# Kernel optimization log

Hardware: AMD Instinct MI355X
Metric: run time of the kernel (lower is better)

Reference implementation:

```python
import math
import jax, jax.numpy as jnp
import numpy as np

B, S, D, H, HD = 32, 512, 768, 12, 64
K, ST = 2, 2  # pooling kernel / stride
NEG = jnp.float32(-10000.0)


def _alibi_slopes(n):
    def p2(m):
        start = 2 ** (-(2 ** (-(math.log2(m) - 3))))
        return [start * start ** i for i in range(m)]
    if math.log2(n).is_integer():
        return p2(n)
    c = 2 ** math.floor(math.log2(n))
    return p2(c) + _alibi_slopes(2 * c)[0::2][: n - c]


def _sum_pool(x, k, s, out_len):
    # x: [B, L, C]; ceil_mode sum-pool over axis 1 (zero padded on the right)
    pad = (out_len - 1) * s + k - x.shape[1]
    if pad > 0:
        x = jnp.pad(x, ((0, 0), (0, pad), (0, 0)))
    win = x[:, jnp.arange(out_len)[:, None] * s + jnp.arange(k)]  # [B, out, k, C]
    return win.sum(axis=2)


def setup_inputs() -> dict:
    key = jax.random.key(0)
    k1, k2, k3 = jax.random.split(key, 3)
    hidden_states = jax.random.normal(k1, (B, S, D), dtype=jnp.float32)
    lengths = jax.random.randint(k2, (B,), 128, S + 1)
    attention_mask = jnp.arange(S)[None, :] < lengths[:, None]  # bool [B,S]
    Wqkv_w = jax.random.normal(k3, (3 * D, D), dtype=jnp.float32) * 0.02
    Wqkv_b = jnp.zeros((3 * D,), dtype=jnp.float32)
    return {"hidden_states": hidden_states, "attention_mask": attention_mask,
            "Wqkv_w": Wqkv_w, "Wqkv_b": Wqkv_b}


def reference(hidden_states, attention_mask, Wqkv_w, Wqkv_b):
    b, s = attention_mask.shape
    qkv = hidden_states @ Wqkv_w.T + Wqkv_b  # [B,S,3D]
    qkv = qkv.reshape(b, s, 3, H, HD)        # '(t h d)' split order
    q = qkv[:, :, 0]                          # [B,S,H,HD]
    k = qkv[:, :, 1].transpose(0, 2, 1, 3)    # [B,H,S,HD]
    v = qkv[:, :, 2].transpose(0, 2, 1, 3)

    # MaskedAvgPool1d on queries (flattened heads), ceil_mode sum-pool / count
    kk = min(K, s)
    out_len = -(-(max(0, s - kk)) // ST) + 1
    q_flat = q.reshape(b, s, H * HD)
    q_flat = jnp.where(attention_mask[:, :, None], q_flat, 0.0)
    norm = _sum_pool(attention_mask.astype(jnp.float32)[:, :, None], kk, ST, out_len)  # [B,out,1]
    new_mask = norm[..., 0] != 0
    norm = jnp.where(norm == 0, 1.0, norm)
    q_pool = _sum_pool(q_flat, kk, ST, out_len) / norm  # [B,out,D]
    q = q_pool.reshape(b, out_len, H, HD).transpose(0, 2, 1, 3)  # [B,H,out,HD]

    # bias: 0 where (new_mask_q & mask_k), else -10000; plus ALiBi
    pair = new_mask[:, :, None] & attention_mask[:, None, :]  # [B,out,S]
    bias = jnp.where(pair, 0.0, NEG)[:, None, :, :]           # [B,1,out,S]
    rel = jnp.abs(jnp.arange(s)[None, :] - jnp.arange(out_len)[:, None])  # [out,S]
    slopes = jnp.asarray(_alibi_slopes(H), dtype=jnp.float32)
    alibi = slopes[:, None, None] * (-rel.astype(jnp.float32))  # [H,out,S]
    scores = jnp.einsum('bhqd,bhkd->bhqk', q, k) / math.sqrt(HD) + bias + alibi[None]
    attn = jax.nn.softmax(scores, axis=-1)
    out = jnp.einsum('bhqk,bhkd->bhqd', attn, v)  # [B,H,out,HD]
    out = out.transpose(0, 2, 1, 3).reshape(b, out_len, H * HD)
    return out, new_mask
```

## Files before the change

### kernel.cpp

```cpp
#include <hip/hip_runtime.h>

#define BB 32
#define SS 512
#define DD 768
#define HH 12
#define HDIM 64
#define OL 256
#define NQKV 2304
#define GM (BB*SS)

#define NEG2 (-14426.9504089f)

typedef __bf16 bf16_t;
typedef bf16_t bf16x8 __attribute__((ext_vector_type(8)));
typedef float f32x4 __attribute__((ext_vector_type(4)));
typedef unsigned short u16x8 __attribute__((ext_vector_type(8)));

__device__ __forceinline__ unsigned short f2bf(float f) {
  unsigned u = __float_as_uint(f);
  u = u + 0x7FFFu + ((u >> 16) & 1u);
  return (unsigned short)(u >> 16);
}
__device__ __forceinline__ float b2f(unsigned short s) {
  return __uint_as_float(((unsigned)s) << 16);
}

__global__ void conv_f32_bf16(const float* __restrict__ in,
                              unsigned short* __restrict__ out, int n4) {
  int i = blockIdx.x * blockDim.x + threadIdx.x;
  if (i >= n4) return;
  float4 v = ((const float4*)in)[i];
  ushort4 o;
  o.x = f2bf(v.x); o.y = f2bf(v.y); o.z = f2bf(v.z); o.w = f2bf(v.w);
  ((ushort4*)out)[i] = o;
}

__global__ void prep_mask(const void* __restrict__ mraw,
                          float* __restrict__ kbias,
                          float* __restrict__ invn,
                          unsigned char* __restrict__ nmask,
                          float* __restrict__ out_nm) {
  int b = blockIdx.x, t = threadIdx.x;
  const unsigned char* mb = (const unsigned char*)mraw;
  bool isbyte = (mb[1] != 0);
  int idx = b * SS + t;
  int mv = isbyte ? (int)(mb[idx] != 0) : (int)(((const int*)mraw)[idx] != 0);
  kbias[idx] = mv ? 0.f : NEG2;
  if (t < OL) {
    int i0 = b * SS + 2 * t, i1 = i0 + 1;
    int m0 = isbyte ? (int)(mb[i0] != 0) : (int)(((const int*)mraw)[i0] != 0);
    int m1 = isbyte ? (int)(mb[i1] != 0) : (int)(((const int*)mraw)[i1] != 0);
    int n = m0 + m1;
    invn[b * OL + t] = (n > 0) ? 1.f / (float)n : 1.f;
    nmask[b * OL + t] = (n > 0) ? 1 : 0;
    out_nm[b * OL + t] = (n > 0) ? 1.f : 0.f;
  }
}

#define NT 12
__global__ __launch_bounds__(256, 2) void gemm_qkv(
    const unsigned short* __restrict__ A,
    const unsigned short* __restrict__ Bt,
    const float* __restrict__ bias,
    unsigned short* __restrict__ Kbuf,
    unsigned short* __restrict__ qp,
    unsigned short* __restrict__ vT,
    const float* __restrict__ kbias,
    const float* __restrict__ invn) {
  __shared__ __align__(16) char smem[65536];

  const int t = threadIdx.x;
  const int lane = t & 63;
  const int w = t >> 6;
  const int wm = w >> 1, wn = w & 1;
  const int fr = lane & 15, hi = lane >> 4;

  const int p = blockIdx.x;
  const int l = (p & 7) * 288 + (p >> 3);
  const int m0 = (l / 18) * 128;
  const int n0 = (l % 18) * 128;
  const int b = m0 >> 9;
  const int s0 = m0 & 511;

  f32x4 acc[4][4] = {};

  const int sr8 = lane >> 3;
  const int sx8 = ((lane & 7) ^ sr8) * 8;
  const int wq = __builtin_amdgcn_readfirstlane(w);
  const unsigned short* aSrc = A + (size_t)(m0 + wq * 32 + sr8) * DD + sx8;
  const unsigned short* bSrc = Bt + (size_t)(n0 + wq * 32 + sr8) * DD + sx8;

#define GLOAD(SRC, DST)                                                        \
  __builtin_amdgcn_global_load_lds(                                           \
      (const __attribute__((address_space(1))) unsigned int*)(SRC),           \
      (__attribute__((address_space(3))) unsigned int*)(DST), 16, 0, 0)

#define STAGE(T) do {                                                          \
    char* da_ = smem + ((T) & 1) * 32768;                                      \
    char* db_ = da_ + 16384;                                                   \
    const unsigned short* as_ = aSrc + (T) * 64;                               \
    const unsigned short* bs_ = bSrc + (T) * 64;                               \
    _Pragma("unroll")                                                          \
    for (int i_ = 0; i_ < 4; ++i_) {                                           \
      GLOAD(as_ + (size_t)i_ * 8 * DD, da_ + (wq * 32 + i_ * 8) * 128);        \
      GLOAD(bs_ + (size_t)i_ * 8 * DD, db_ + (wq * 32 + i_ * 8) * 128);        \
    }                                                                          \
  } while (0)

  STAGE(0);
  STAGE(1);

  const int cb0 = (hi * 16) ^ ((fr & 7) << 4);
  const int cb1 = (64 + hi * 16) ^ ((fr & 7) << 4);

  for (int kt = 0; kt < NT; ++kt) {
    if (kt < NT - 1) {
      asm volatile("s_waitcnt vmcnt(8)" ::: "memory");
    } else {
      asm volatile("s_waitcnt vmcnt(0)" ::: "memory");
    }
    __builtin_amdgcn_sched_barrier(0);
    __builtin_amdgcn_s_barrier();
    __builtin_amdgcn_sched_barrier(0);

    const char* bA = smem + (kt & 1) * 32768;
    const char* bB = bA + 16384;

    bf16x8 a0[4], b0[4], a1[4], b1[4];
#pragma unroll
    for (int f = 0; f < 4; ++f) {
      a0[f] = *(const bf16x8*)(bA + (wm * 64 + f * 16 + fr) * 128 + cb0);
      b0[f] = *(const bf16x8*)(bB + (wn * 64 + f * 16 + fr) * 128 + cb0);
    }
    __builtin_amdgcn_sched_barrier(0);
#pragma unroll
    for (int f = 0; f < 4; ++f) {
      a1[f] = *(const bf16x8*)(bA + (wm * 64 + f * 16 + fr) * 128 + cb1);
      b1[f] = *(const bf16x8*)(bB + (wn * 64 + f * 16 + fr) * 128 + cb1);
    }
    asm volatile("s_waitcnt lgkmcnt(8)" ::: "memory");
    __builtin_amdgcn_sched_barrier(0);
    __builtin_amdgcn_s_setprio(1);
#pragma unroll
    for (int mf = 0; mf < 4; ++mf)
#pragma unroll
      for (int nf = 0; nf < 4; ++nf)
        acc[mf][nf] = __builtin_amdgcn_mfma_f32_16x16x32_bf16(
            a0[mf], b0[nf], acc[mf][nf], 0, 0, 0);
    __builtin_amdgcn_s_setprio(0);
    asm volatile("s_waitcnt lgkmcnt(0)" ::: "memory");
    __builtin_amdgcn_sched_barrier(0);
    __builtin_amdgcn_s_barrier();
    __builtin_amdgcn_sched_barrier(0);
    if (kt + 2 < NT) STAGE(kt + 2);
    __builtin_amdgcn_sched_barrier(0);
    __builtin_amdgcn_s_setprio(1);
#pragma unroll
    for (int mf = 0; mf < 4; ++mf)
#pragma unroll
      for (int nf = 0; nf < 4; ++nf)
        acc[mf][nf] = __builtin_amdgcn_mfma_f32_16x16x32_bf16(
            a1[mf], b1[nf], acc[mf][nf], 0, 0, 0);
    __builtin_amdgcn_s_setprio(0);
  }
#undef STAGE
#undef GLOAD

  const int ntype = n0 / 768;
  if (ntype == 1) {
#pragma unroll
    for (int nf = 0; nf < 4; ++nf) {
      const int nc = wn * 64 + nf * 16 + fr;
      const float bvs = bias[n0 + nc];
      const int gnc = n0 - 768 + nc;
#pragma unroll
      for (int mf = 0; mf < 4; ++mf) {
        const int gmr = m0 + wm * 64 + mf * 16 + hi * 4;
#pragma unroll
        for (int j = 0; j < 4; ++j)
          Kbuf[(size_t)(gmr + j) * 768 + gnc] = f2bf(acc[mf][nf][j] + bvs);
      }
    }
  } else if (ntype == 0) {
#pragma unroll
    for (int mf = 0; mf < 4; ++mf) {
      const int sl = s0 + wm * 64 + mf * 16 + hi * 4;
      const float4 km = *(const float4*)&kbias[b * SS + sl];
      const float2 iv = *(const float2*)&invn[b * OL + (sl >> 1)];
      const float w0 = (km.x == 0.f) ? iv.x : 0.f;
      const float w1 = (km.y == 0.f) ? iv.x : 0.f;
      const float w2 = (km.z == 0.f) ? iv.y : 0.f;
      const float w3 = (km.w == 0.f) ? iv.y : 0.f;
      const int o0 = b * OL + (sl >> 1);
#pragma unroll
      for (int nf = 0; nf < 4; ++nf) {
        const int gnc = n0 + wn * 64 + nf * 16 + fr;
        const float bvs = bias[gnc];
        const f32x4 a = acc[mf][nf];
        qp[(size_t)o0 * DD + gnc] = f2bf((a[0] + bvs) * w0 + (a[1] + bvs) * w1);
        qp[(size_t)(o0 + 1) * DD + gnc] = f2bf((a[2] + bvs) * w2 + (a[3] + bvs) * w3);
      }
    }
  } else {
    unsigned short* lt = (unsigned short*)smem;
#pragma unroll
    for (int nf = 0; nf < 4; ++nf) {
      const int nl = wn * 64 + nf * 16 + fr;
      const float bvs = bias[n0 + nl];
#pragma unroll
      for (int mf = 0; mf < 4; ++mf) {
        const int mb = wm * 64 + mf * 16 + hi * 4;
        ushort4 pk;
        pk.x = f2bf(acc[mf][nf][0] + bvs);
        pk.y = f2bf(acc[mf][nf][1] + bvs);
        pk.z = f2bf(acc[mf][nf][2] + bvs);
        pk.w = f2bf(acc[mf][nf][3] + bvs);
        *(ushort4*)&lt[nl * 136 + mb] = pk;
      }
    }
    __syncthreads();
#pragma unroll
    for (int i = 0; i < 8; ++i) {
      const int row = i * 16 + (t >> 4);
      const int ch = t & 15;
      const u16x8 v = *(const u16x8*)&lt[row * 136 + ch * 8];
      const int n = n0 - 1536 + row;
      const int h2 = n >> 6, d2 = n & 63;
      *(u16x8*)(vT + ((size_t)((b * HH + h2) * HDIM + d2)) * 512 + s0 + ch * 8) = v;
    }
  }
}

__constant__ float c_slopes2[12] = {
    0.72134752f, 0.36067376f, 0.18033688f, 0.09016844f,
    0.04508422f, 0.02254211f, 0.011271055f, 0.0056355275f,
    1.02013945f, 0.51006972f, 0.25503486f, 0.12751743f};

__global__ __launch_bounds__(256) void attn_mfma(
    const unsigned short* __restrict__ qp,
    const unsigned short* __restrict__ Kb,
    const unsigned short* __restrict__ vT,
    const float* __restrict__ kbias,
    const unsigned char* __restrict__ nmask,
    float* __restrict__ out) {
  __shared__ __align__(16) char smem[51200];
  const int t = threadIdx.x;
  const int lane = t & 63;
  const int w = t >> 6;
  const int wq = __builtin_amdgcn_readfirstlane(w);
  const int fr = lane & 15, hi = lane >> 4;

  const int p = blockIdx.x;
  const int l = (p & 7) * 96 + (p >> 3);
  const int qb = l & 1;
  const int bh = l >> 1;
  const int h = bh % HH, b = bh / HH;
  const int q0 = qb * 128 + wq * 32;

  char* ptb = smem + 32768 + wq * 4096;
  float* kbl = (float*)(smem + 49152);

  const int srow = lane >> 3;
  const int scol = ((lane & 7) ^ srow) * 8;

#define GLOAD(SRC, DST)                                                        \
  __builtin_amdgcn_global_load_lds(                                           \
      (const __attribute__((address_space(1))) unsigned int*)(SRC),           \
      (__attribute__((address_space(3))) unsigned int*)(DST), 16, 0, 0)

  if (wq == 0) {
    GLOAD(kbias + b * SS + lane * 4, smem + 49152);
    GLOAD(kbias + b * SS + 256 + lane * 4, smem + 50176);
  }

  bf16x8 qf[2][2];
#pragma unroll
  for (int m = 0; m < 2; ++m)
#pragma unroll
    for (int ks = 0; ks < 2; ++ks)
      qf[m][ks] = *(const bf16x8*)(qp + (size_t)(b * OL + q0 + m * 16 + fr) * DD +
                                   h * HDIM + ks * 32 + hi * 8);

  int nmv = (int)nmask[b * OL + q0 + (lane & 31)];
  int qmbits = 0;
#pragma unroll
  for (int m = 0; m < 2; ++m)
#pragma unroll
    for (int j = 0; j < 4; ++j)
      if (__shfl(nmv, m * 16 + hi * 4 + j, 64)) qmbits |= 1 << (m * 4 + j);

  const float slope2 = c_slopes2[h];
  f32x4 oacc[2][4] = {};
  float lpart[2][4] = {};

#define STAGE(TILE, BUF) do {                                                  \
    char* kd_ = smem + (BUF) * 8192 + wq * 2048;                               \
    char* vd_ = smem + 16384 + (BUF) * 8192 + wq * 2048;                       \
    const unsigned short* ks_ =                                                \
        Kb + (size_t)(b * SS + (TILE) * 64 + wq * 16 + srow) * 768 + h * HDIM + scol; \
    const unsigned short* vs_ =                                                \
        vT + (size_t)((b * HH + h) * HDIM + wq * 16 + srow) * SS + (TILE) * 64 + scol; \
    GLOAD(ks_, kd_);                                                           \
    GLOAD(ks_ + (size_t)8 * 768, kd_ + 1024);                                  \
    GLOAD(vs_, vd_);                                                           \
    GLOAD(vs_ + (size_t)8 * SS, vd_ + 1024);                                   \
  } while (0)

  __builtin_amdgcn_sched_barrier(0);
  STAGE(0, 0);
  STAGE(1, 1);
  __builtin_amdgcn_sched_barrier(0);

  for (int tile = 0; tile < 8; ++tile) {
    const int cur = tile & 1;
    const int key0 = tile * 64;
    if (tile < 7) {
      asm volatile("s_waitcnt vmcnt(4)" ::: "memory");
    } else {
      asm volatile("s_waitcnt vmcnt(0)" ::: "memory");
    }
    __builtin_amdgcn_sched_barrier(0);
    __builtin_amdgcn_s_barrier();
    __builtin_amdgcn_sched_barrier(0);

    char* ktb = smem + cur * 8192;
    char* vtb = smem + 16384 + cur * 8192;

    f32x4 sacc[2][4] = {};
#pragma unroll
    for (int ks = 0; ks < 2; ++ks) {
      bf16x8 kf[4];
#pragma unroll
      for (int n = 0; n < 4; ++n) {
        const int by = ((n * 16 + fr) * 128 + (ks * 64 + hi * 16)) ^ ((fr & 7) << 4);
        kf[n] = *(const bf16x8*)(ktb + by);
      }
#pragma unroll
      for (int m = 0; m < 2; ++m)
#pragma unroll
        for (int n = 0; n < 4; ++n)
          sacc[m][n] = __builtin_amdgcn_mfma_f32_16x16x32_bf16(qf[m][ks], kf[n], sacc[m][n], 0, 0, 0);
    }

    float kbv[4], keyfv[4];
#pragma unroll
    for (int n = 0; n < 4; ++n) {
      kbv[n] = kbl[key0 + n * 16 + fr];
      keyfv[n] = (float)(key0 + n * 16 + fr);
    }
#pragma unroll
    for (int m = 0; m < 2; ++m) {
#pragma unroll
      for (int j = 0; j < 4; ++j) {
        const bool qm = (qmbits >> (m * 4 + j)) & 1;
        const float qvf = (float)(q0 + m * 16 + hi * 4 + j);
        float lp = lpart[m][j];
#pragma unroll
        for (int n = 0; n < 4; ++n) {
          const float biasv = qm ? kbv[n] : 0.f;
          const float rel = fabsf(keyfv[n] - qvf);
          float tv = fmaf(sacc[m][n][j], 0.18033688011f, biasv);
          tv = fmaf(rel, -slope2, tv);
          float pe;
          asm("v_exp_f32 %0, %1" : "=v"(pe) : "v"(tv));
          lp += pe;
          const int by = ((m * 16 + hi * 4 + j) * 128 + (n * 16 + fr) * 2) ^
                         (((hi * 4 + j) & 7) << 4);
          *(unsigned short*)(ptb + by) = f2bf(pe);
        }
        lpart[m][j] = lp;
      }
    }
    asm volatile("s_waitcnt lgkmcnt(0)" ::: "memory");
    __builtin_amdgcn_sched_barrier(0);

#pragma unroll
    for (int ks = 0; ks < 2; ++ks) {
      bf16x8 pf[2], vf[4];
#pragma unroll
      for (int m = 0; m < 2; ++m) {
        const int by = ((m * 16 + fr) * 128 + (ks * 64 + hi * 16)) ^ ((fr & 7) << 4);
        pf[m] = *(const bf16x8*)(ptb + by);
      }
#pragma unroll
      for (int nd = 0; nd < 4; ++nd) {
        const int by = ((nd * 16 + fr) * 128 + (ks * 64 + hi * 16)) ^ ((fr & 7) << 4);
        vf[nd] = *(const bf16x8*)(vtb + by);
      }
#pragma unroll
      for (int m = 0; m < 2; ++m)
#pragma unroll
        for (int nd = 0; nd < 4; ++nd)
          oacc[m][nd] = __builtin_amdgcn_mfma_f32_16x16x32_bf16(pf[m], vf[nd], oacc[m][nd], 0, 0, 0);
    }

    __builtin_amdgcn_sched_barrier(0);
    __builtin_amdgcn_s_barrier();
    __builtin_amdgcn_sched_barrier(0);
    if (tile + 2 < 8) STAGE(tile + 2, cur);
  }
#undef STAGE
#undef GLOAD

  float* ot = (float*)(smem + wq * 8704);
#pragma unroll
  for (int m = 0; m < 2; ++m)
#pragma unroll
    for (int j = 0; j < 4; ++j) {
      float lv = lpart[m][j];
      lv += __shfl_xor(lv, 1, 64);
      lv += __shfl_xor(lv, 2, 64);
      lv += __shfl_xor(lv, 4, 64);
      lv += __shfl_xor(lv, 8, 64);
      const float rl = 1.f / lv;
      const int row = m * 16 + hi * 4 + j;
#pragma unroll
      for (int nd = 0; nd < 4; ++nd)
        ot[row * 68 + nd * 16 + fr] = oacc[m][nd][j] * rl;
    }
  asm volatile("s_waitcnt lgkmcnt(0)" ::: "memory");
  __builtin_amdgcn_sched_barrier(0);
#pragma unroll
  for (int i = 0; i < 8; ++i) {
    const int idx = i * 64 + lane;
    const int row = idx >> 4, c4 = idx & 15;
    const float4 v = *(const float4*)&ot[row * 68 + c4 * 4];
    *(float4*)(out + (size_t)(b * OL + q0 + row) * DD + h * HDIM + c4 * 4) = v;
  }
}

extern "C" void kernel_launch(void* const* d_in, const int* in_sizes, int n_in,
                              void* d_out, int out_size, void* d_ws, size_t ws_size,
                              hipStream_t stream) {
  const float* hidden = (const float*)d_in[0];
  const void* maskraw = d_in[1];
  const float* W = (const float*)d_in[2];
  const float* bias = (const float*)d_in[3];
  float* out = (float*)d_out;

  char* ws = (char*)d_ws;
  unsigned short* Abf  = (unsigned short*)(ws);
  unsigned short* Btb  = (unsigned short*)(ws + 25165824);
  unsigned short* Kbuf = (unsigned short*)(ws + 28704768);
  unsigned short* vT   = (unsigned short*)(ws + 53870592);
  unsigned short* qp   = (unsigned short*)(ws + 79036416);
  float* kbias         = (float*)(ws + 91619328);
  float* invn          = (float*)(ws + 91684864);
  unsigned char* nmask = (unsigned char*)(ws + 91717632);

  float* out_nm = out + (size_t)BB * OL * DD;

  conv_f32_bf16<<<(GM * DD / 4 + 255) / 256, 256, 0, stream>>>(hidden, Abf, GM * DD / 4);
  conv_f32_bf16<<<(NQKV * DD / 4 + 255) / 256, 256, 0, stream>>>(W, Btb, NQKV * DD / 4);
  prep_mask<<<BB, SS, 0, stream>>>(maskraw, kbias, invn, nmask, out_nm);
  gemm_qkv<<<2304, 256, 0, stream>>>(Abf, Btb, bias, Kbuf, qp, vT, kbias, invn);
  attn_mfma<<<768, 256, 0, stream>>>(qp, Kbuf, vT, kbias, nmask, out);
}
```

Before: 112.3 us.

## Enlarge QKV GEMM tile to 128x256 with 8 waves and triple-buffered LDS

The QKV projection GEMM now uses 512-thread blocks, each computing a 128x256 output tile with a 2x4 wave grid, so half as many blocks are launched. Global-to-LDS staging moves from double to triple buffering across 144 KB of shared memory. Each K-step's loads are split into two halves interleaved between the MFMA phases, with waits tuned to match. The goal is better operand reuse per loaded byte and better overlap of memory traffic with MFMA work. In exchange, the large LDS footprint likely limits residency to one block per CU, and tile-level parallelism drops.

```diff
diff --git a/kernel.cpp b/kernel.cpp
--- a/kernel.cpp
+++ b/kernel.cpp
@@ -57,8 +57,7 @@
   }
 }
 
-#define NT 12
-__global__ __launch_bounds__(256, 2) void gemm_qkv(
+__global__ __launch_bounds__(512, 2) void gemm_qkv(
     const unsigned short* __restrict__ A,
     const unsigned short* __restrict__ Bt,
     const float* __restrict__ bias,
@@ -67,18 +66,19 @@
     unsigned short* __restrict__ vT,
     const float* __restrict__ kbias,
     const float* __restrict__ invn) {
-  __shared__ __align__(16) char smem[65536];
+  __shared__ __align__(16) char smem[147456];
 
   const int t = threadIdx.x;
   const int lane = t & 63;
   const int w = t >> 6;
-  const int wm = w >> 1, wn = w & 1;
+  const int wm = w >> 2;
+  const int wn = w & 3;
   const int fr = lane & 15, hi = lane >> 4;
 
   const int p = blockIdx.x;
-  const int l = (p & 7) * 288 + (p >> 3);
-  const int m0 = (l / 18) * 128;
-  const int n0 = (l % 18) * 128;
+  const int l = (p & 7) * 144 + (p >> 3);
+  const int m0 = (l / 9) * 128;
+  const int n0 = (l % 9) * 256;
   const int b = m0 >> 9;
   const int s0 = m0 & 511;
 
@@ -87,87 +87,111 @@
   const int sr8 = lane >> 3;
   const int sx8 = ((lane & 7) ^ sr8) * 8;
   const int wq = __builtin_amdgcn_readfirstlane(w);
-  const unsigned short* aSrc = A + (size_t)(m0 + wq * 32 + sr8) * DD + sx8;
-  const unsigned short* bSrc = Bt + (size_t)(n0 + wq * 32 + sr8) * DD + sx8;
+  const unsigned short* aS = A + (size_t)(m0 + wq * 16 + sr8) * DD + sx8;
+  const unsigned short* bS = Bt + (size_t)(n0 + wq * 32 + sr8) * DD + sx8;
 
 #define GLOAD(SRC, DST)                                                        \
   __builtin_amdgcn_global_load_lds(                                           \
       (const __attribute__((address_space(1))) unsigned int*)(SRC),           \
       (__attribute__((address_space(3))) unsigned int*)(DST), 16, 0, 0)
 
-#define STAGE(T) do {                                                          \
-    char* da_ = smem + ((T) & 1) * 32768;                                      \
-    char* db_ = da_ + 16384;                                                   \
-    const unsigned short* as_ = aSrc + (T) * 64;                               \
-    const unsigned short* bs_ = bSrc + (T) * 64;                               \
+#define STG_A(KT, SB, Q) GLOAD(aS + (size_t)(8 * (Q)) * DD + (KT) * 64,        \
+                               (SB) + (wq * 16 + 8 * (Q)) * 128)
+#define STG_B(KT, SB, Q) GLOAD(bS + (size_t)(8 * (Q)) * DD + (KT) * 64,        \
+                               (SB) + 16384 + (wq * 32 + 8 * (Q)) * 128)
+#define STG_H1(KT, SB) do { STG_A(KT, SB, 0); STG_A(KT, SB, 1); STG_B(KT, SB, 0); } while (0)
+#define STG_H2(KT, SB) do { STG_B(KT, SB, 1); STG_B(KT, SB, 2); STG_B(KT, SB, 3); } while (0)
+
+#define SBAR()                                                                 \
+  do {                                                                         \
+    __builtin_amdgcn_sched_barrier(0);                                         \
+    __builtin_amdgcn_s_barrier();                                              \
+    __builtin_amdgcn_sched_barrier(0);                                         \
+  } while (0)
+
+#define MFMA16(AF, BF)                                                         \
+  do {                                                                         \
+    asm volatile("s_waitcnt lgkmcnt(0)" ::: "memory");                          \
+    __builtin_amdgcn_sched_barrier(0);                                         \
+    __builtin_amdgcn_s_setprio(1);                                             \
     _Pragma("unroll")                                                          \
-    for (int i_ = 0; i_ < 4; ++i_) {                                           \
-      GLOAD(as_ + (size_t)i_ * 8 * DD, da_ + (wq * 32 + i_ * 8) * 128);        \
-      GLOAD(bs_ + (size_t)i_ * 8 * DD, db_ + (wq * 32 + i_ * 8) * 128);        \
-    }                                                                          \
+    for (int mf_ = 0; mf_ < 4; ++mf_)                                          \
+      _Pragma("unroll")                                                        \
+      for (int nf_ = 0; nf_ < 4; ++nf_)                                        \
+        acc[mf_][nf_] = __builtin_amdgcn_mfma_f32_16x16x32_bf16(               \
+            (AF)[mf_], (BF)[nf_], acc[mf_][nf_], 0, 0, 0);                     \
+    __builtin_amdgcn_s_setprio(0);                                             \
   } while (0)
-
-  STAGE(0);
-  STAGE(1);
 
   const int cb0 = (hi * 16) ^ ((fr & 7) << 4);
   const int cb1 = (64 + hi * 16) ^ ((fr & 7) << 4);
-
-  for (int kt = 0; kt < NT; ++kt) {
-    if (kt < NT - 1) {
-      asm volatile("s_waitcnt vmcnt(8)" ::: "memory");
+  const int arow = (wm * 64 + fr) * 128;
+  const int brow = 16384 + (wn * 64 + fr) * 128;
+
+  STG_H1(0, smem); STG_H2(0, smem);
+  STG_H1(1, smem + 49152); STG_H2(1, smem + 49152);
+
+  int se = 0;
+#pragma unroll
+  for (int it = 0; it < 6; ++it) {
+    char* sE = smem + se * 49152;
+    char* sO = smem + (se == 2 ? 0 : se + 1) * 49152;
+    char* dE = smem + (se == 0 ? 2 : se - 1) * 49152;
+    char* dO = sE;
+    const int ke = 2 * it + 2, ko = 2 * it + 3;
+
+    bf16x8 af[4], bf[4];
+
+    asm volatile("s_waitcnt vmcnt(6)" ::: "memory");
+    SBAR();
+#pragma unroll
+    for (int f = 0; f < 4; ++f) af[f] = *(const bf16x8*)(sE + arow + f * 2048 + cb0);
+#pragma unroll
+    for (int f = 0; f < 4; ++f) bf[f] = *(const bf16x8*)(sE + brow + f * 2048 + cb0);
+    if (it < 5) STG_H1(ke, dE);
+    MFMA16(af, bf);
+
+    SBAR();
+#pragma unroll
+    for (int f = 0; f < 4; ++f) af[f] = *(const bf16x8*)(sE + arow + f * 2048 + cb1);
+#pragma unroll
+    for (int f = 0; f < 4; ++f) bf[f] = *(const bf16x8*)(sE + brow + f * 2048 + cb1);
+    if (it < 5) STG_H2(ke, dE);
+    MFMA16(af, bf);
+
+    if (it < 5) {
+      asm volatile("s_waitcnt vmcnt(6)" ::: "memory");
     } else {
       asm volatile("s_waitcnt vmcnt(0)" ::: "memory");
     }
-    __builtin_amdgcn_sched_barrier(0);
-    __builtin_amdgcn_s_barrier();
-    __builtin_amdgcn_sched_barrier(0);
-
-    const char* bA = smem + (kt & 1) * 32768;
-    const char* bB = bA + 16384;
-
-    bf16x8 a0[4], b0[4], a1[4], b1[4];
-#pragma unroll
-    for (int f = 0; f < 4; ++f) {
-      a0[f] = *(const bf16x8*)(bA + (wm * 64 + f * 16 + fr) * 128 + cb0);
-      b0[f] = *(const bf16x8*)(bB + (wn * 64 + f * 16 + fr) * 128 + cb0);
-    }
-    __builtin_amdgcn_sched_barrier(0);
-#pragma unroll
-    for (int f = 0; f < 4; ++f) {
-      a1[f] = *(const bf16x8*)(bA + (wm * 64 + f * 16 + fr) * 128 + cb1);
-      b1[f] = *(const bf16x8*)(bB + (wn * 64 + f * 16 + fr) * 128 + cb1);
-    }
-    asm volatile("s_waitcnt lgkmcnt(8)" ::: "memory");
-    __builtin_amdgcn_sched_barrier(0);
-    __builtin_amdgcn_s_setprio(1);
-#pragma unroll
-    for (int mf = 0; mf < 4; ++mf)
-#pragma unroll
-      for (int nf = 0; nf < 4; ++nf)
-        acc[mf][nf] = __builtin_amdgcn_mfma_f32_16x16x32_bf16(
-            a0[mf], b0[nf], acc[mf][nf], 0, 0, 0);
-    __builtin_amdgcn_s_setprio(0);
-    asm volatile("s_waitcnt lgkmcnt(0)" ::: "memory");
-    __builtin_amdgcn_sched_barrier(0);
-    __builtin_amdgcn_s_barrier();
-    __builtin_amdgcn_sched_barrier(0);
-    if (kt + 2 < NT) STAGE(kt + 2);
-    __builtin_amdgcn_sched_barrier(0);
-    __builtin_amdgcn_s_setprio(1);
-#pragma unroll
-    for (int mf = 0; mf < 4; ++mf)
-#pragma unroll
-      for (int nf = 0; nf < 4; ++nf)
-        acc[mf][nf] = __builtin_amdgcn_mfma_f32_16x16x32_bf16(
-            a1[mf], b1[nf], acc[mf][nf], 0, 0, 0);
-    __builtin_amdgcn_s_setprio(0);
-  }
-#undef STAGE
+    SBAR();
+#pragma unroll
+    for (int f = 0; f < 4; ++f) af[f] = *(const bf16x8*)(sO + arow + f * 2048 + cb0);
+#pragma unroll
+    for (int f = 0; f < 4; ++f) bf[f] = *(const bf16x8*)(sO + brow + f * 2048 + cb0);
+    if (it < 5) STG_H1(ko, dO);
+    MFMA16(af, bf);
+
+    SBAR();
+#pragma unroll
+    for (int f = 0; f < 4; ++f) af[f] = *(const bf16x8*)(sO + arow + f * 2048 + cb1);
+#pragma unroll
+    for (int f = 0; f < 4; ++f) bf[f] = *(const bf16x8*)(sO + brow + f * 2048 + cb1);
+    if (it < 5) STG_H2(ko, dO);
+    MFMA16(af, bf);
+
+    se = (se + 2) % 3;
+  }
+#undef STG_A
+#undef STG_B
+#undef STG_H1
+#undef STG_H2
+#undef MFMA16
+#undef SBAR
 #undef GLOAD
 
-  const int ntype = n0 / 768;
-  if (ntype == 1) {
+  const int nt = n0 / 768;
+  if (nt == 1) {
 #pragma unroll
     for (int nf = 0; nf < 4; ++nf) {
       const int nc = wn * 64 + nf * 16 + fr;
@@ -181,7 +205,7 @@
           Kbuf[(size_t)(gmr + j) * 768 + gnc] = f2bf(acc[mf][nf][j] + bvs);
       }
     }
-  } else if (ntype == 0) {
+  } else if (nt == 0) {
 #pragma unroll
     for (int mf = 0; mf < 4; ++mf) {
       const int sl = s0 + wm * 64 + mf * 16 + hi * 4;
@@ -209,23 +233,24 @@
       const float bvs = bias[n0 + nl];
 #pragma unroll
       for (int mf = 0; mf < 4; ++mf) {
-        const int mb = wm * 64 + mf * 16 + hi * 4;
+        const int ml = wm * 64 + mf * 16 + hi * 4;
         ushort4 pk;
         pk.x = f2bf(acc[mf][nf][0] + bvs);
         pk.y = f2bf(acc[mf][nf][1] + bvs);
         pk.z = f2bf(acc[mf][nf][2] + bvs);
         pk.w = f2bf(acc[mf][nf][3] + bvs);
-        *(ushort4*)&lt[nl * 136 + mb] = pk;
+        *(ushort4*)&lt[nl * 136 + ml] = pk;
       }
     }
     __syncthreads();
 #pragma unroll
     for (int i = 0; i < 8; ++i) {
-      const int row = i * 16 + (t >> 4);
-      const int ch = t & 15;
-      const u16x8 v = *(const u16x8*)&lt[row * 136 + ch * 8];
-      const int n = n0 - 1536 + row;
-      const int h2 = n >> 6, d2 = n & 63;
+      const int task = i * 512 + t;
+      const int r = task >> 4;
+      const int ch = task & 15;
+      const u16x8 v = *(const u16x8*)&lt[r * 136 + ch * 8];
+      const int nv = n0 - 1536 + r;
+      const int h2 = nv >> 6, d2 = nv & 63;
       *(u16x8*)(vT + ((size_t)((b * HH + h2) * HDIM + d2)) * 512 + s0 + ch * 8) = v;
     }
   }
@@ -453,6 +478,6 @@
   conv_f32_bf16<<<(GM * DD / 4 + 255) / 256, 256, 0, stream>>>(hidden, Abf, GM * DD / 4);
   conv_f32_bf16<<<(NQKV * DD / 4 + 255) / 256, 256, 0, stream>>>(W, Btb, NQKV * DD / 4);
   prep_mask<<<BB, SS, 0, stream>>>(maskraw, kbias, invn, nmask, out_nm);
-  gemm_qkv<<<2304, 256, 0, stream>>>(Abf, Btb, bias, Kbuf, qp, vT, kbias, invn);
+  gemm_qkv<<<1152, 512, 0, stream>>>(Abf, Btb, bias, Kbuf, qp, vT, kbias, invn);
   attn_mfma<<<768, 256, 0, stream>>>(qp, Kbuf, vT, kbias, nmask, out);
 }
```

After: 114.8 us. 2.2% more time.

## Enlarge QKV GEMM tile to 256x256 with 8 waves and per-wave V transpose

Applied to the files above, without the earlier changes.

The QKV projection GEMM moves from 128x128 tiles with 4 waves to 256x256 tiles with 8 waves (512 threads, 128KB LDS double buffer). Each wave now computes 128x64, which raises arithmetic intensity and cuts global/LDS traffic per FLOP. The V-transpose epilogue is redone per wave through a private LDS tile, so it no longer needs a block-wide sync. In exchange the grid drops to 576 blocks and there is more register pressure (32 accumulators), which may lower occupancy and hurt load balance across CUs. With 128KB of LDS per block, the __launch_bounds__(512, 2) hint likely cannot be met, so probably only one block fits per CU.

```diff
diff --git a/kernel.cpp b/kernel.cpp
--- a/kernel.cpp
+++ b/kernel.cpp
@@ -57,8 +57,7 @@
   }
 }
 
-#define NT 12
-__global__ __launch_bounds__(256, 2) void gemm_qkv(
+__global__ __launch_bounds__(512, 2) void gemm_qkv(
     const unsigned short* __restrict__ A,
     const unsigned short* __restrict__ Bt,
     const float* __restrict__ bias,
@@ -67,54 +66,80 @@
     unsigned short* __restrict__ vT,
     const float* __restrict__ kbias,
     const float* __restrict__ invn) {
-  __shared__ __align__(16) char smem[65536];
+  __shared__ __align__(16) char smem[131072];
 
   const int t = threadIdx.x;
   const int lane = t & 63;
   const int w = t >> 6;
-  const int wm = w >> 1, wn = w & 1;
+  const int wm = w >> 2;
+  const int wn = w & 3;
   const int fr = lane & 15, hi = lane >> 4;
 
   const int p = blockIdx.x;
-  const int l = (p & 7) * 288 + (p >> 3);
-  const int m0 = (l / 18) * 128;
-  const int n0 = (l % 18) * 128;
+  const int l = (p & 7) * 72 + (p >> 3);
+  const int m0 = (l / 9) * 256;
+  const int n0 = (l % 9) * 256;
   const int b = m0 >> 9;
   const int s0 = m0 & 511;
 
-  f32x4 acc[4][4] = {};
+  f32x4 acc[8][4] = {};
 
   const int sr8 = lane >> 3;
   const int sx8 = ((lane & 7) ^ sr8) * 8;
   const int wq = __builtin_amdgcn_readfirstlane(w);
-  const unsigned short* aSrc = A + (size_t)(m0 + wq * 32 + sr8) * DD + sx8;
-  const unsigned short* bSrc = Bt + (size_t)(n0 + wq * 32 + sr8) * DD + sx8;
+  const unsigned short* aS = A + (size_t)(m0 + wq * 32 + sr8) * DD + sx8;
+  const unsigned short* bS = Bt + (size_t)(n0 + wq * 32 + sr8) * DD + sx8;
 
 #define GLOAD(SRC, DST)                                                        \
   __builtin_amdgcn_global_load_lds(                                           \
       (const __attribute__((address_space(1))) unsigned int*)(SRC),           \
       (__attribute__((address_space(3))) unsigned int*)(DST), 16, 0, 0)
 
-#define STAGE(T) do {                                                          \
-    char* da_ = smem + ((T) & 1) * 32768;                                      \
-    char* db_ = da_ + 16384;                                                   \
-    const unsigned short* as_ = aSrc + (T) * 64;                               \
-    const unsigned short* bs_ = bSrc + (T) * 64;                               \
+#define STAGE(KT, BUF) do {                                                    \
+    char* da_ = (BUF);                                                         \
+    char* db_ = (BUF) + 32768;                                                 \
+    const unsigned short* as_ = aS + (KT) * 64;                                \
+    const unsigned short* bs_ = bS + (KT) * 64;                                \
     _Pragma("unroll")                                                          \
-    for (int i_ = 0; i_ < 4; ++i_) {                                           \
-      GLOAD(as_ + (size_t)i_ * 8 * DD, da_ + (wq * 32 + i_ * 8) * 128);        \
-      GLOAD(bs_ + (size_t)i_ * 8 * DD, db_ + (wq * 32 + i_ * 8) * 128);        \
+    for (int q_ = 0; q_ < 4; ++q_) {                                           \
+      GLOAD(as_ + (size_t)(8 * q_) * DD, da_ + (wq * 32 + 8 * q_) * 128);      \
+      GLOAD(bs_ + (size_t)(8 * q_) * DD, db_ + (wq * 32 + 8 * q_) * 128);      \
     }                                                                          \
   } while (0)
 
-  STAGE(0);
-  STAGE(1);
+#define MFMA32()                                                               \
+  do {                                                                         \
+    asm volatile("s_waitcnt lgkmcnt(0)" ::: "memory");                          \
+    __builtin_amdgcn_sched_barrier(0);                                         \
+    __builtin_amdgcn_s_setprio(1);                                             \
+    _Pragma("unroll")                                                          \
+    for (int mf_ = 0; mf_ < 8; ++mf_)                                          \
+      _Pragma("unroll")                                                        \
+      for (int nf_ = 0; nf_ < 4; ++nf_)                                        \
+        acc[mf_][nf_] = __builtin_amdgcn_mfma_f32_16x16x32_bf16(               \
+            af[mf_], bf[nf_], acc[mf_][nf_], 0, 0, 0);                         \
+    __builtin_amdgcn_s_setprio(0);                                             \
+  } while (0)
+
+#define RD(SB, CB)                                                             \
+  do {                                                                         \
+    _Pragma("unroll")                                                          \
+    for (int f_ = 0; f_ < 8; ++f_)                                             \
+      af[f_] = *(const bf16x8*)((SB) + (wm * 128 + f_ * 16 + fr) * 128 + (CB)); \
+    _Pragma("unroll")                                                          \
+    for (int f_ = 0; f_ < 4; ++f_)                                             \
+      bf[f_] = *(const bf16x8*)((SB) + 32768 + (wn * 64 + f_ * 16 + fr) * 128 + (CB)); \
+  } while (0)
 
   const int cb0 = (hi * 16) ^ ((fr & 7) << 4);
   const int cb1 = (64 + hi * 16) ^ ((fr & 7) << 4);
 
-  for (int kt = 0; kt < NT; ++kt) {
-    if (kt < NT - 1) {
+  STAGE(0, smem);
+  STAGE(1, smem + 65536);
+
+#pragma unroll 2
+  for (int kt = 0; kt < 12; ++kt) {
+    if (kt < 11) {
       asm volatile("s_waitcnt vmcnt(8)" ::: "memory");
     } else {
       asm volatile("s_waitcnt vmcnt(0)" ::: "memory");
@@ -123,68 +148,52 @@
     __builtin_amdgcn_s_barrier();
     __builtin_amdgcn_sched_barrier(0);
 
-    const char* bA = smem + (kt & 1) * 32768;
-    const char* bB = bA + 16384;
-
-    bf16x8 a0[4], b0[4], a1[4], b1[4];
-#pragma unroll
-    for (int f = 0; f < 4; ++f) {
-      a0[f] = *(const bf16x8*)(bA + (wm * 64 + f * 16 + fr) * 128 + cb0);
-      b0[f] = *(const bf16x8*)(bB + (wn * 64 + f * 16 + fr) * 128 + cb0);
-    }
-    __builtin_amdgcn_sched_barrier(0);
-#pragma unroll
-    for (int f = 0; f < 4; ++f) {
-      a1[f] = *(const bf16x8*)(bA + (wm * 64 + f * 16 + fr) * 128 + cb1);
-      b1[f] = *(const bf16x8*)(bB + (wn * 64 + f * 16 + fr) * 128 + cb1);
-    }
-    asm volatile("s_waitcnt lgkmcnt(8)" ::: "memory");
+    char* bA = smem + (kt & 1) * 65536;
+    bf16x8 af[8], bf[4];
+
+    RD(bA, cb0);
+    MFMA32();
+
+    RD(bA, cb1);
+    asm volatile("s_waitcnt lgkmcnt(0)" ::: "memory");
+    __builtin_amdgcn_sched_barrier(0);
+    __builtin_amdgcn_s_barrier();
+    __builtin_amdgcn_sched_barrier(0);
+    if (kt + 2 < 12) STAGE(kt + 2, bA);
     __builtin_amdgcn_sched_barrier(0);
     __builtin_amdgcn_s_setprio(1);
 #pragma unroll
-    for (int mf = 0; mf < 4; ++mf)
+    for (int mf = 0; mf < 8; ++mf)
 #pragma unroll
       for (int nf = 0; nf < 4; ++nf)
         acc[mf][nf] = __builtin_amdgcn_mfma_f32_16x16x32_bf16(
-            a0[mf], b0[nf], acc[mf][nf], 0, 0, 0);
+            af[mf], bf[nf], acc[mf][nf], 0, 0, 0);
     __builtin_amdgcn_s_setprio(0);
-    asm volatile("s_waitcnt lgkmcnt(0)" ::: "memory");
-    __builtin_amdgcn_sched_barrier(0);
-    __builtin_amdgcn_s_barrier();
-    __builtin_amdgcn_sched_barrier(0);
-    if (kt + 2 < NT) STAGE(kt + 2);
-    __builtin_amdgcn_sched_barrier(0);
-    __builtin_amdgcn_s_setprio(1);
-#pragma unroll
-    for (int mf = 0; mf < 4; ++mf)
-#pragma unroll
-      for (int nf = 0; nf < 4; ++nf)
-        acc[mf][nf] = __builtin_amdgcn_mfma_f32_16x16x32_bf16(
-            a1[mf], b1[nf], acc[mf][nf], 0, 0, 0);
-    __builtin_amdgcn_s_setprio(0);
-  }
+  }
+#undef RD
+#undef MFMA32
 #undef STAGE
 #undef GLOAD
 
-  const int ntype = n0 / 768;
-  if (ntype == 1) {
+  const int nt = n0 / 768;
+  if (nt == 1) {
 #pragma unroll
     for (int nf = 0; nf < 4; ++nf) {
       const int nc = wn * 64 + nf * 16 + fr;
       const float bvs = bias[n0 + nc];
       const int gnc = n0 - 768 + nc;
 #pragma unroll
-      for (int mf = 0; mf < 4; ++mf) {
-        const int gmr = m0 + wm * 64 + mf * 16 + hi * 4;
+      for (int mf = 0; mf < 8; ++mf) {
+        const int gmr = m0 + wm * 128 + mf * 16 + hi * 4;
 #pragma unroll
         for (int j = 0; j < 4; ++j)
           Kbuf[(size_t)(gmr + j) * 768 + gnc] = f2bf(acc[mf][nf][j] + bvs);
       }
     }
-  } else if (ntype == 0) {
-#pragma unroll
-    for (int mf = 0; mf < 4; ++mf) {
-      const int sl = s0 + wm * 64 + mf * 16 + hi * 4;
+  } else if (nt == 0) {
+#pragma unroll
+    for (int mf = 0; mf < 8; ++mf) {
+      const int sl = s0 + wm * 128 + mf * 16 + hi * 4;
       const float4 km = *(const float4*)&kbias[b * SS + sl];
       const float2 iv = *(const float2*)&invn[b * OL + (sl >> 1)];
       const float w0 = (km.x == 0.f) ? iv.x : 0.f;
@@ -202,31 +211,39 @@
       }
     }
   } else {
-    unsigned short* lt = (unsigned short*)smem;
-#pragma unroll
-    for (int nf = 0; nf < 4; ++nf) {
-      const int nl = wn * 64 + nf * 16 + fr;
-      const float bvs = bias[n0 + nl];
-#pragma unroll
-      for (int mf = 0; mf < 4; ++mf) {
-        const int mb = wm * 64 + mf * 16 + hi * 4;
-        ushort4 pk;
-        pk.x = f2bf(acc[mf][nf][0] + bvs);
-        pk.y = f2bf(acc[mf][nf][1] + bvs);
-        pk.z = f2bf(acc[mf][nf][2] + bvs);
-        pk.w = f2bf(acc[mf][nf][3] + bvs);
-        *(ushort4*)&lt[nl * 136 + mb] = pk;
-      }
-    }
-    __syncthreads();
-#pragma unroll
-    for (int i = 0; i < 8; ++i) {
-      const int row = i * 16 + (t >> 4);
-      const int ch = t & 15;
-      const u16x8 v = *(const u16x8*)&lt[row * 136 + ch * 8];
-      const int n = n0 - 1536 + row;
-      const int h2 = n >> 6, d2 = n & 63;
-      *(u16x8*)(vT + ((size_t)((b * HH + h2) * HDIM + d2)) * 512 + s0 + ch * 8) = v;
+    const int h2 = ((n0 - 1536) >> 6) + wn;
+    unsigned short* tile = (unsigned short*)(smem + wq * 9216);
+    float bvs[4];
+#pragma unroll
+    for (int nf = 0; nf < 4; ++nf) bvs[nf] = bias[n0 + wn * 64 + nf * 16 + fr];
+#pragma unroll
+    for (int mh = 0; mh < 2; ++mh) {
+#pragma unroll
+      for (int nf = 0; nf < 4; ++nf) {
+        const int d = nf * 16 + fr;
+#pragma unroll
+        for (int mf2 = 0; mf2 < 4; ++mf2) {
+          const int mf = mh * 4 + mf2;
+          ushort4 pk;
+          pk.x = f2bf(acc[mf][nf][0] + bvs[nf]);
+          pk.y = f2bf(acc[mf][nf][1] + bvs[nf]);
+          pk.z = f2bf(acc[mf][nf][2] + bvs[nf]);
+          pk.w = f2bf(acc[mf][nf][3] + bvs[nf]);
+          *(ushort4*)&tile[d * 72 + mf2 * 16 + hi * 4] = pk;
+        }
+      }
+      asm volatile("s_waitcnt lgkmcnt(0)" ::: "memory");
+      __builtin_amdgcn_sched_barrier(0);
+      const int sb = s0 + wm * 128 + mh * 64;
+#pragma unroll
+      for (int i = 0; i < 8; ++i) {
+        const int task = i * 64 + lane;
+        const int d = task >> 3, ch = task & 7;
+        const u16x8 v = *(const u16x8*)&tile[d * 72 + ch * 8];
+        *(u16x8*)(vT + ((size_t)((b * HH + h2) * HDIM + d)) * 512 + sb + ch * 8) = v;
+      }
+      asm volatile("s_waitcnt lgkmcnt(0)" ::: "memory");
+      __builtin_amdgcn_sched_barrier(0);
     }
   }
 }
@@ -453,6 +470,6 @@
   conv_f32_bf16<<<(GM * DD / 4 + 255) / 256, 256, 0, stream>>>(hidden, Abf, GM * DD / 4);
   conv_f32_bf16<<<(NQKV * DD / 4 + 255) / 256, 256, 0, stream>>>(W, Btb, NQKV * DD / 4);
   prep_mask<<<BB, SS, 0, stream>>>(maskraw, kbias, invn, nmask, out_nm);
-  gemm_qkv<<<2304, 256, 0, stream>>>(Abf, Btb, bias, Kbuf, qp, vT, kbias, invn);
+  gemm_qkv<<<576, 512, 0, stream>>>(Abf, Btb, bias, Kbuf, qp, vT, kbias, invn);
   attn_mfma<<<768, 256, 0, stream>>>(qp, Kbuf, vT, kbias, nmask, out);
 }
```

After: 141.9 us, median of 2. 1.26x slower.

## Pool hidden states before Q projection to halve the query GEMM work

Applied to the files above, without the earlier changes.

The masked average pooling is applied to the bf16 hidden states before projection, using linearity, instead of pooling projected queries. The Q part of the QKV GEMM then runs over 256 pooled rows per batch instead of 512, cutting the tile grid from 2304 to 1920 blocks. The fp32-to-bf16 conversion of hidden states is merged into the new pool_conv kernel, which also writes the pooled activations. Bias is added after pooling and gated by the new mask; the pooled values are rounded to bf16 before the GEMM, which slightly changes numerics.

```diff
diff --git a/kernel.cpp b/kernel.cpp
--- a/kernel.cpp
+++ b/kernel.cpp
@@ -57,16 +57,44 @@
   }
 }
 
+__global__ void pool_conv(const float* __restrict__ hidden,
+                          const float* __restrict__ kbias,
+                          const float* __restrict__ invn,
+                          unsigned short* __restrict__ Abf,
+                          unsigned short* __restrict__ Apool) {
+  int i = blockIdx.x * blockDim.x + threadIdx.x;
+  if (i >= BB * OL * (DD / 4)) return;
+  const int c = (i % 192) * 4;
+  const int ol = i / 192;
+  const int b = ol >> 8, o = ol & 255;
+  const int s0 = b * SS + 2 * o;
+  const float4 h0 = *(const float4*)(hidden + (size_t)s0 * DD + c);
+  const float4 h1 = *(const float4*)(hidden + (size_t)(s0 + 1) * DD + c);
+  ushort4 a0, a1, ap;
+  a0.x = f2bf(h0.x); a0.y = f2bf(h0.y); a0.z = f2bf(h0.z); a0.w = f2bf(h0.w);
+  a1.x = f2bf(h1.x); a1.y = f2bf(h1.y); a1.z = f2bf(h1.z); a1.w = f2bf(h1.w);
+  const float m0v = (kbias[s0] == 0.f) ? 1.f : 0.f;
+  const float m1v = (kbias[s0 + 1] == 0.f) ? 1.f : 0.f;
+  const float inv = invn[ol];
+  ap.x = f2bf((h0.x * m0v + h1.x * m1v) * inv);
+  ap.y = f2bf((h0.y * m0v + h1.y * m1v) * inv);
+  ap.z = f2bf((h0.z * m0v + h1.z * m1v) * inv);
+  ap.w = f2bf((h0.w * m0v + h1.w * m1v) * inv);
+  *(ushort4*)(Abf + (size_t)s0 * DD + c) = a0;
+  *(ushort4*)(Abf + (size_t)(s0 + 1) * DD + c) = a1;
+  *(ushort4*)(Apool + (size_t)ol * DD + c) = ap;
+}
+
 #define NT 12
 __global__ __launch_bounds__(256, 2) void gemm_qkv(
     const unsigned short* __restrict__ A,
+    const unsigned short* __restrict__ Apool,
     const unsigned short* __restrict__ Bt,
     const float* __restrict__ bias,
     unsigned short* __restrict__ Kbuf,
     unsigned short* __restrict__ qp,
     unsigned short* __restrict__ vT,
-    const float* __restrict__ kbias,
-    const float* __restrict__ invn) {
+    const unsigned char* __restrict__ nmask) {
   __shared__ __align__(16) char smem[65536];
 
   const int t = threadIdx.x;
@@ -76,18 +104,19 @@
   const int fr = lane & 15, hi = lane >> 4;
 
   const int p = blockIdx.x;
-  const int l = (p & 7) * 288 + (p >> 3);
-  const int m0 = (l / 18) * 128;
-  const int n0 = (l % 18) * 128;
-  const int b = m0 >> 9;
-  const int s0 = m0 & 511;
+  const int l = (p & 7) * 240 + (p >> 3);
+  const bool isQ = l >= 1536;
+  int m0, n0;
+  if (!isQ) { m0 = (l / 12) * 128; n0 = 768 + (l % 12) * 128; }
+  else      { const int l2 = l - 1536; m0 = (l2 / 6) * 128; n0 = (l2 % 6) * 128; }
+  const unsigned short* Asel = isQ ? Apool : A;
 
   f32x4 acc[4][4] = {};
 
   const int sr8 = lane >> 3;
   const int sx8 = ((lane & 7) ^ sr8) * 8;
   const int wq = __builtin_amdgcn_readfirstlane(w);
-  const unsigned short* aSrc = A + (size_t)(m0 + wq * 32 + sr8) * DD + sx8;
+  const unsigned short* aSrc = Asel + (size_t)(m0 + wq * 32 + sr8) * DD + sx8;
   const unsigned short* bSrc = Bt + (size_t)(n0 + wq * 32 + sr8) * DD + sx8;
 
 #define GLOAD(SRC, DST)                                                        \
@@ -166,8 +195,27 @@
 #undef STAGE
 #undef GLOAD
 
-  const int ntype = n0 / 768;
-  if (ntype == 1) {
+  if (isQ) {
+#pragma unroll
+    for (int mf = 0; mf < 4; ++mf) {
+      const int r0 = m0 + wm * 64 + mf * 16 + hi * 4;
+      const uchar4 nm = *(const uchar4*)&nmask[r0];
+      const float g0 = nm.x ? 1.f : 0.f;
+      const float g1 = nm.y ? 1.f : 0.f;
+      const float g2 = nm.z ? 1.f : 0.f;
+      const float g3 = nm.w ? 1.f : 0.f;
+#pragma unroll
+      for (int nf = 0; nf < 4; ++nf) {
+        const int gnc = n0 + wn * 64 + nf * 16 + fr;
+        const float bvs = bias[gnc];
+        const f32x4 a = acc[mf][nf];
+        qp[(size_t)(r0 + 0) * 768 + gnc] = f2bf((a[0] + bvs) * g0);
+        qp[(size_t)(r0 + 1) * 768 + gnc] = f2bf((a[1] + bvs) * g1);
+        qp[(size_t)(r0 + 2) * 768 + gnc] = f2bf((a[2] + bvs) * g2);
+        qp[(size_t)(r0 + 3) * 768 + gnc] = f2bf((a[3] + bvs) * g3);
+      }
+    }
+  } else if (n0 < 1536) {
 #pragma unroll
     for (int nf = 0; nf < 4; ++nf) {
       const int nc = wn * 64 + nf * 16 + fr;
@@ -181,27 +229,9 @@
           Kbuf[(size_t)(gmr + j) * 768 + gnc] = f2bf(acc[mf][nf][j] + bvs);
       }
     }
-  } else if (ntype == 0) {
-#pragma unroll
-    for (int mf = 0; mf < 4; ++mf) {
-      const int sl = s0 + wm * 64 + mf * 16 + hi * 4;
-      const float4 km = *(const float4*)&kbias[b * SS + sl];
-      const float2 iv = *(const float2*)&invn[b * OL + (sl >> 1)];
-      const float w0 = (km.x == 0.f) ? iv.x : 0.f;
-      const float w1 = (km.y == 0.f) ? iv.x : 0.f;
-      const float w2 = (km.z == 0.f) ? iv.y : 0.f;
-      const float w3 = (km.w == 0.f) ? iv.y : 0.f;
-      const int o0 = b * OL + (sl >> 1);
-#pragma unroll
-      for (int nf = 0; nf < 4; ++nf) {
-        const int gnc = n0 + wn * 64 + nf * 16 + fr;
-        const float bvs = bias[gnc];
-        const f32x4 a = acc[mf][nf];
-        qp[(size_t)o0 * DD + gnc] = f2bf((a[0] + bvs) * w0 + (a[1] + bvs) * w1);
-        qp[(size_t)(o0 + 1) * DD + gnc] = f2bf((a[2] + bvs) * w2 + (a[3] + bvs) * w3);
-      }
-    }
   } else {
+    const int b = m0 >> 9;
+    const int s0 = m0 & 511;
     unsigned short* lt = (unsigned short*)smem;
 #pragma unroll
     for (int nf = 0; nf < 4; ++nf) {
@@ -439,20 +469,21 @@
   float* out = (float*)d_out;
 
   char* ws = (char*)d_ws;
-  unsigned short* Abf  = (unsigned short*)(ws);
-  unsigned short* Btb  = (unsigned short*)(ws + 25165824);
-  unsigned short* Kbuf = (unsigned short*)(ws + 28704768);
-  unsigned short* vT   = (unsigned short*)(ws + 53870592);
-  unsigned short* qp   = (unsigned short*)(ws + 79036416);
-  float* kbias         = (float*)(ws + 91619328);
-  float* invn          = (float*)(ws + 91684864);
-  unsigned char* nmask = (unsigned char*)(ws + 91717632);
+  unsigned short* Abf   = (unsigned short*)(ws);
+  unsigned short* Btb   = (unsigned short*)(ws + 25165824);
+  unsigned short* Kbuf  = (unsigned short*)(ws + 28704768);
+  unsigned short* vT    = (unsigned short*)(ws + 53870592);
+  unsigned short* qp    = (unsigned short*)(ws + 79036416);
+  float* kbias          = (float*)(ws + 91619328);
+  float* invn           = (float*)(ws + 91684864);
+  unsigned char* nmask  = (unsigned char*)(ws + 91717632);
+  unsigned short* Apool = (unsigned short*)(ws + 91725824);
 
   float* out_nm = out + (size_t)BB * OL * DD;
 
-  conv_f32_bf16<<<(GM * DD / 4 + 255) / 256, 256, 0, stream>>>(hidden, Abf, GM * DD / 4);
   conv_f32_bf16<<<(NQKV * DD / 4 + 255) / 256, 256, 0, stream>>>(W, Btb, NQKV * DD / 4);
   prep_mask<<<BB, SS, 0, stream>>>(maskraw, kbias, invn, nmask, out_nm);
-  gemm_qkv<<<2304, 256, 0, stream>>>(Abf, Btb, bias, Kbuf, qp, vT, kbias, invn);
+  pool_conv<<<(BB * OL * (DD / 4) + 255) / 256, 256, 0, stream>>>(hidden, kbias, invn, Abf, Apool);
+  gemm_qkv<<<1920, 256, 0, stream>>>(Abf, Apool, Btb, bias, Kbuf, qp, vT, nmask);
   attn_mfma<<<768, 256, 0, stream>>>(qp, Kbuf, vT, kbias, nmask, out);
 }
```

Measured after the change: 107.3 us. 4.5% less time.
